# Kernel tuning notes

Hardware: AMD Instinct MI355X
Metric: run time of the kernel (lower is better)

The kernel has to match this reference:

```python
import jax, jax.numpy as jnp
import numpy as np

NEG_BIG = -9e15
ALPHA = 0.2  # LeakyReLU negative slope


def setup_inputs() -> dict:
    key = jax.random.key(0)
    k1, k2, k3, k4 = jax.random.split(key, 4)
    B, N, Fin, Fout = 4, 2048, 128, 128
    h = jax.random.normal(k1, (B, N, Fin), dtype=jnp.float32)
    adj = jax.random.randint(k2, (N, N), 0, 2, dtype=jnp.int32)
    W = jax.random.normal(k3, (Fin, Fout), dtype=jnp.float32) * 0.1
    a = jax.random.normal(k4, (2 * Fout, 1), dtype=jnp.float32) * 0.1
    return {"h": h, "adj": adj, "W": W, "a": a}


def reference(h, adj, W, a):
    # Wh: [B, N, Fout]
    Wh = jnp.einsum('bnf,fo->bno', h, W)
    Fout = W.shape[1]
    a1 = a[:Fout, 0]   # attends to source i
    a2 = a[Fout:, 0]   # attends to target j
    # Decomposed form of leakyrelu(cat([Wh_i, Wh_j]) @ a):
    # e_ij = leakyrelu(a1.Wh_i + a2.Wh_j)  -> [B, N, N]
    f1 = Wh @ a1  # [B, N]
    f2 = Wh @ a2  # [B, N]
    e = jax.nn.leaky_relu(f1[:, :, None] + f2[:, None, :], negative_slope=ALPHA)
    attention = jnp.where(adj[None, :, :] > 0, e, jnp.float32(NEG_BIG))
    attention = jax.nn.softmax(attention, axis=2)
    # dropout is identity in eval mode
    h_prime = jnp.einsum('bij,bjo->bio', attention, Wh)
    return h_prime
```

## Files before the change

### kernel.cpp

```cpp
#include <hip/hip_runtime.h>

#define BB 4
#define NN 2048
#define FF 128
#define NP 2176
#define ALPHA 0.2f
#define SHIFT_C 16.0f

typedef short bf16x8 __attribute__((ext_vector_type(8)));
typedef float f32x4 __attribute__((ext_vector_type(4)));
typedef unsigned u32;

__device__ inline short f2bf(float f) {
    union { float f; unsigned u; } v; v.f = f;
    unsigned r = (v.u + 0x7FFFu + ((v.u >> 16) & 1u)) >> 16;
    return (short)r;
}
__device__ inline float bf2f(short s) {
    union { float f; unsigned u; } v;
    v.u = ((unsigned)(unsigned short)s) << 16;
    return v.f;
}

__device__ inline void cp16(const void* g, void* l) {
    __builtin_amdgcn_global_load_lds(
        (const __attribute__((address_space(1))) u32*)g,
        (__attribute__((address_space(3))) u32*)l, 16, 0, 0);
}

__global__ __launch_bounds__(256) void k_wh(const float* __restrict__ h,
                                            const float* __restrict__ W,
                                            const float* __restrict__ a,
                                            const int* __restrict__ adj,
                                            short* __restrict__ WhHiT,
                                            short* __restrict__ WhLoT,
                                            float* __restrict__ f1,
                                            float* __restrict__ f2,
                                            u32* __restrict__ adjp) {
    __shared__ float Wa[2 * FF];
    __shared__ float hs[16 * 128];
    int tid = threadIdx.x;
    int r0 = blockIdx.x * 16;

    {
        int fin = tid & 127;
        const float* av = (tid < 128) ? a : (a + FF);
        const float* wr = W + (size_t)fin * FF;
        float s = 0.f;
        for (int o = 0; o < FF; o += 4) {
            float4 wv = *(const float4*)(wr + o);
            float4 avv = *(const float4*)(av + o);
            s += wv.x * avv.x + wv.y * avv.y + wv.z * avv.z + wv.w * avv.w;
        }
        Wa[(tid < 128 ? 0 : FF) + fin] = s;
    }
    {
        const float4* src = (const float4*)(h + (size_t)r0 * FF);
        float4* dst = (float4*)hs;
        dst[tid] = src[tid];
        dst[256 + tid] = src[256 + tid];
    }
    {
        int g = blockIdx.x * 256 + tid;
        int row = g >> 6, wd = g & 63;
        const int4* ar = (const int4*)(adj + (size_t)row * NN + wd * 32);
        u32 word = 0;
#pragma unroll
        for (int q = 0; q < 8; ++q) {
            int4 v = ar[q];
            word |= (u32)(v.x > 0) << (q * 4);
            word |= (u32)(v.y > 0) << (q * 4 + 1);
            word |= (u32)(v.z > 0) << (q * 4 + 2);
            word |= (u32)(v.w > 0) << (q * 4 + 3);
        }
        adjp[row * 64 + wd] = word;
    }
    __syncthreads();

    {
        int w = tid >> 6, lane = tid & 63;
        float wa1_0 = Wa[lane], wa1_1 = Wa[lane + 64];
        float wa2_0 = Wa[FF + lane], wa2_1 = Wa[FF + lane + 64];
        for (int rr = 0; rr < 4; ++rr) {
            int rloc = w * 4 + rr;
            int row = r0 + rloc;
            float x0 = hs[rloc * FF + lane], x1 = hs[rloc * FF + lane + 64];
            float s1 = x0 * wa1_0 + x1 * wa1_1;
            float s2 = x0 * wa2_0 + x1 * wa2_1;
#pragma unroll
            for (int m = 32; m >= 1; m >>= 1) {
                s1 += __shfl_xor(s1, m, 64);
                s2 += __shfl_xor(s2, m, 64);
            }
            if (lane == 0) { f1[row] = s1; f2[row] = s2; }
        }
    }

    int f4 = (tid & 31) * 4;
    int rg = tid >> 5;
    float acc[2][4];
#pragma unroll
    for (int rr = 0; rr < 2; ++rr)
#pragma unroll
        for (int cc = 0; cc < 4; ++cc) acc[rr][cc] = 0.f;

    for (int k0 = 0; k0 < FF; k0 += 4) {
        float4 wv[4];
#pragma unroll
        for (int kk = 0; kk < 4; ++kk)
            wv[kk] = *(const float4*)(W + (size_t)(k0 + kk) * FF + f4);
        float4 hv[2];
#pragma unroll
        for (int rr = 0; rr < 2; ++rr)
            hv[rr] = *(const float4*)(hs + (rg * 2 + rr) * FF + k0);
#pragma unroll
        for (int rr = 0; rr < 2; ++rr) {
            float hk[4] = {hv[rr].x, hv[rr].y, hv[rr].z, hv[rr].w};
#pragma unroll
            for (int kk = 0; kk < 4; ++kk) {
                acc[rr][0] += hk[kk] * wv[kk].x;
                acc[rr][1] += hk[kk] * wv[kk].y;
                acc[rr][2] += hk[kk] * wv[kk].z;
                acc[rr][3] += hk[kk] * wv[kk].w;
            }
        }
    }
    int rloc = r0 + rg * 2;
    int b = rloc >> 11;
    int j = rloc & (NN - 1);
#pragma unroll
    for (int cc = 0; cc < 4; ++cc) {
        float v0 = acc[0][cc], v1 = acc[1][cc];
        short h0 = f2bf(v0), h1 = f2bf(v1);
        short l0 = f2bf(v0 - bf2f(h0)), l1 = f2bf(v1 - bf2f(h1));
        size_t off = (size_t)(b * FF + f4 + cc) * NP + j;
        *(short2*)(WhHiT + off) = make_short2(h0, h1);
        *(short2*)(WhLoT + off) = make_short2(l0, l1);
    }
}

__global__ __launch_bounds__(512, 4) void k_attn(const short* __restrict__ WhHiT,
                                                 const short* __restrict__ WhLoT,
                                                 const u32* __restrict__ adjp,
                                                 const float* __restrict__ f1,
                                                 const float* __restrict__ f2,
                                                 float* __restrict__ out) {
    __shared__ __align__(16) char lds[44160];
    char* Bb = lds;
    char* Ab = lds + 32768;
    float* row_ps = (float*)(lds + 43008);
    float* row_inv = (float*)(lds + 44032);

    int tid = threadIdx.x;
    int w = tid >> 6, lane = tid & 63;
    int blk = blockIdx.x;
    int b = blk >> 7;
    int tile = (blk >> 1) & 63;
    int half = blk & 1;
    int i0 = tile * 32;

    int r_a = lane & 15, kg = lane >> 4;
    int mi = w >> 2, ni = w & 3;

    int rb = tid & 31;
    int jp = (tid >> 5) & 15;
    float f1i = f1[b * NN + i0 + rb];
    const u32* aprow = adjp + (size_t)(i0 + rb) * 64;
    const float* f2b = f2 + b * NN;
    int aoff = (rb >> 4) * 1280 + (rb & 15) * 80 + jp * 4;

    int isLo = w >> 2;
    int sub = w & 3;
    int fo_s = half * 64 + sub * 16 + (lane >> 2);
    int oc_s = lane & 3;
    const short* gB = (isLo ? WhLoT : WhHiT) + (size_t)(b * FF + fo_s) * NP + oc_s * 8;
    int bB = isLo * 4096 + sub * 1024;

    f32x4 acc = {0.f, 0.f, 0.f, 0.f};
    float sp = 0.f;

    cp16(gB, Bb + bB);
    cp16(gB + 32, Bb + 8192 + bB);
    {
        float2 qa = *(const float2*)(f2b + jp * 2);
        float2 qb = *(const float2*)(f2b + 32 + jp * 2);
        u32 wa = aprow[0], wb = aprow[1];
        float x;
        x = f1i + qa.x; x = fmaxf(x, ALPHA * x);
        float p00 = __expf(x - SHIFT_C) * (float)((wa >> (jp * 2)) & 1u);
        x = f1i + qa.y; x = fmaxf(x, ALPHA * x);
        float p01 = __expf(x - SHIFT_C) * (float)((wa >> (jp * 2 + 1)) & 1u);
        x = f1i + qb.x; x = fmaxf(x, ALPHA * x);
        float p10 = __expf(x - SHIFT_C) * (float)((wb >> (jp * 2)) & 1u);
        x = f1i + qb.y; x = fmaxf(x, ALPHA * x);
        float p11 = __expf(x - SHIFT_C) * (float)((wb >> (jp * 2 + 1)) & 1u);
        sp += p00 + p01 + p10 + p11;
        union { float f; u32 u; } u0, u1;
        u0.f = p00; u1.f = p01;
        *(u32*)(Ab + aoff) = ((u0.u + 0x8000u) >> 16) | (((u1.u + 0x8000u) >> 16) << 16);
        u0.f = p10; u1.f = p11;
        *(u32*)(Ab + 2560 + aoff) = ((u0.u + 0x8000u) >> 16) | (((u1.u + 0x8000u) >> 16) << 16);
    }
    float2 pfa = *(const float2*)(f2b + 64 + jp * 2);
    float2 pfb = *(const float2*)(f2b + 96 + jp * 2);
    u32 pwa = aprow[2], pwb = aprow[3];
    __syncthreads();

    for (int p = 0; p < 32; ++p) {
        int par = p & 1, opar = par ^ 1;
        {
            int j0n = ((2 * p + 2) & 63) * 32;
            int j1n = ((2 * p + 3) & 63) * 32;
            cp16(gB + j0n, Bb + opar * 16384 + bB);
            cp16(gB + j1n, Bb + opar * 16384 + 8192 + bB);
        }
        {
            float x;
            x = f1i + pfa.x; x = fmaxf(x, ALPHA * x);
            float p00 = __expf(x - SHIFT_C) * (float)((pwa >> (jp * 2)) & 1u);
            x = f1i + pfa.y; x = fmaxf(x, ALPHA * x);
            float p01 = __expf(x - SHIFT_C) * (float)((pwa >> (jp * 2 + 1)) & 1u);
            x = f1i + pfb.x; x = fmaxf(x, ALPHA * x);
            float p10 = __expf(x - SHIFT_C) * (float)((pwb >> (jp * 2)) & 1u);
            x = f1i + pfb.y; x = fmaxf(x, ALPHA * x);
            float p11 = __expf(x - SHIFT_C) * (float)((pwb >> (jp * 2 + 1)) & 1u);
            if (p < 31) sp += p00 + p01 + p10 + p11;
            union { float f; u32 u; } u0, u1;
            u0.f = p00; u1.f = p01;
            *(u32*)(Ab + opar * 5120 + aoff) =
                ((u0.u + 0x8000u) >> 16) | (((u1.u + 0x8000u) >> 16) << 16);
            u0.f = p10; u1.f = p11;
            *(u32*)(Ab + opar * 5120 + 2560 + aoff) =
                ((u0.u + 0x8000u) >> 16) | (((u1.u + 0x8000u) >> 16) << 16);
        }
        {
            int s0 = (2 * p + 4) & 63, s1 = (2 * p + 5) & 63;
            pfa = *(const float2*)(f2b + s0 * 32 + jp * 2);
            pfb = *(const float2*)(f2b + s1 * 32 + jp * 2);
            pwa = aprow[s0]; pwb = aprow[s1];
        }
        {
            char* bbase = Bb + par * 16384;
            char* abase = Ab + par * 5120;
            int boff = (ni * 16 + r_a) * 64 + kg * 16;
            bf16x8 af0 = *(const bf16x8*)(abase + mi * 1280 + r_a * 80 + kg * 16);
            bf16x8 b0h = *(const bf16x8*)(bbase + boff);
            bf16x8 b0l = *(const bf16x8*)(bbase + 4096 + boff);
            acc = __builtin_amdgcn_mfma_f32_16x16x32_bf16(af0, b0h, acc, 0, 0, 0);
            acc = __builtin_amdgcn_mfma_f32_16x16x32_bf16(af0, b0l, acc, 0, 0, 0);
            bf16x8 af1 = *(const bf16x8*)(abase + 2560 + mi * 1280 + r_a * 80 + kg * 16);
            bf16x8 b1h = *(const bf16x8*)(bbase + 8192 + boff);
            bf16x8 b1l = *(const bf16x8*)(bbase + 8192 + 4096 + boff);
            acc = __builtin_amdgcn_mfma_f32_16x16x32_bf16(af1, b1h, acc, 0, 0, 0);
            acc = __builtin_amdgcn_mfma_f32_16x16x32_bf16(af1, b1l, acc, 0, 0, 0);
        }
        __syncthreads();
    }

    sp += __shfl_xor(sp, 32, 64);
    if (lane < 32) row_ps[w * 32 + lane] = sp;
    __syncthreads();
    if (tid < 32) {
        float t = 0.f;
#pragma unroll
        for (int ww = 0; ww < 8; ++ww) t += row_ps[ww * 32 + tid];
        row_inv[tid] = 1.0f / t;
    }
    __syncthreads();

    float* ob = out + ((size_t)b * NN + i0 + mi * 16) * FF + half * 64 + ni * 16;
#pragma unroll
    for (int q = 0; q < 4; ++q) {
        int rr = kg * 4 + q;
        ob[(size_t)rr * FF + r_a] = acc[q] * row_inv[mi * 16 + rr];
    }
}

extern "C" void kernel_launch(void* const* d_in, const int* in_sizes, int n_in,
                              void* d_out, int out_size, void* d_ws, size_t ws_size,
                              hipStream_t stream) {
    const float* h   = (const float*)d_in[0];
    const int*   adj = (const int*)d_in[1];
    const float* W   = (const float*)d_in[2];
    const float* a   = (const float*)d_in[3];
    float* out = (float*)d_out;

    short* WhHiT = (short*)d_ws;
    short* WhLoT = WhHiT + (size_t)BB * FF * NP;
    float* f1 = (float*)(WhLoT + (size_t)BB * FF * NP);
    float* f2 = f1 + (size_t)BB * NN;
    u32* adjp = (u32*)(f2 + (size_t)BB * NN);

    k_wh<<<(BB * NN) / 16, 256, 0, stream>>>(h, W, a, adj, WhHiT, WhLoT, f1, f2, adjp);
    k_attn<<<512, 512, 0, stream>>>(WhHiT, WhLoT, adjp, f1, f2, out);
}
```

Measured before the change: 135.9 us.

## Split MFMA work by K-stage across waves and swizzle B tile LDS layout

Waves are now split by K half (stage) instead of by M row block. Each wave computes both 16-row M blocks for its K half, so every B fragment load feeds two MFMAs, and the two K partial sums are reduced through LDS at the end. The B tile column index is XOR-swizzled on both the global-to-LDS copy and the read side to cut LDS bank conflicts. The cost is an extra accumulator, an LDS partial-sum exchange before the epilogue, and only half the waves doing the output stores.

```diff
diff --git a/kernel.cpp b/kernel.cpp
--- a/kernel.cpp
+++ b/kernel.cpp
@@ -150,6 +150,7 @@
     char* Ab = lds + 32768;
     float* row_ps = (float*)(lds + 43008);
     float* row_inv = (float*)(lds + 44032);
+    float* pP = (float*)lds;
 
     int tid = threadIdx.x;
     int w = tid >> 6, lane = tid & 63;
@@ -160,7 +161,8 @@
     int i0 = tile * 32;
 
     int r_a = lane & 15, kg = lane >> 4;
-    int mi = w >> 2, ni = w & 3;
+    int st = w >> 2, ni = w & 3;
+    int csw = kg ^ ((r_a >> 1) & 3);
 
     int rb = tid & 31;
     int jp = (tid >> 5) & 15;
@@ -172,11 +174,12 @@
     int isLo = w >> 2;
     int sub = w & 3;
     int fo_s = half * 64 + sub * 16 + (lane >> 2);
-    int oc_s = lane & 3;
+    int oc_s = (lane & 3) ^ ((lane >> 3) & 3);
     const short* gB = (isLo ? WhLoT : WhHiT) + (size_t)(b * FF + fo_s) * NP + oc_s * 8;
     int bB = isLo * 4096 + sub * 1024;
 
-    f32x4 acc = {0.f, 0.f, 0.f, 0.f};
+    f32x4 acc0 = {0.f, 0.f, 0.f, 0.f};
+    f32x4 acc1 = {0.f, 0.f, 0.f, 0.f};
     float sp = 0.f;
 
     cp16(gB, Bb + bB);
@@ -240,25 +243,28 @@
             pwa = aprow[s0]; pwb = aprow[s1];
         }
         {
-            char* bbase = Bb + par * 16384;
-            char* abase = Ab + par * 5120;
-            int boff = (ni * 16 + r_a) * 64 + kg * 16;
-            bf16x8 af0 = *(const bf16x8*)(abase + mi * 1280 + r_a * 80 + kg * 16);
-            bf16x8 b0h = *(const bf16x8*)(bbase + boff);
-            bf16x8 b0l = *(const bf16x8*)(bbase + 4096 + boff);
-            acc = __builtin_amdgcn_mfma_f32_16x16x32_bf16(af0, b0h, acc, 0, 0, 0);
-            acc = __builtin_amdgcn_mfma_f32_16x16x32_bf16(af0, b0l, acc, 0, 0, 0);
-            bf16x8 af1 = *(const bf16x8*)(abase + 2560 + mi * 1280 + r_a * 80 + kg * 16);
-            bf16x8 b1h = *(const bf16x8*)(bbase + 8192 + boff);
-            bf16x8 b1l = *(const bf16x8*)(bbase + 8192 + 4096 + boff);
-            acc = __builtin_amdgcn_mfma_f32_16x16x32_bf16(af1, b1h, acc, 0, 0, 0);
-            acc = __builtin_amdgcn_mfma_f32_16x16x32_bf16(af1, b1l, acc, 0, 0, 0);
+            char* bbase = Bb + par * 16384 + st * 8192;
+            char* abase = Ab + par * 5120 + st * 2560;
+            int boff = (ni * 16 + r_a) * 64 + csw * 16;
+            int aoffr = r_a * 80 + kg * 16;
+            bf16x8 a0 = *(const bf16x8*)(abase + aoffr);
+            bf16x8 a1 = *(const bf16x8*)(abase + 1280 + aoffr);
+            bf16x8 bh = *(const bf16x8*)(bbase + boff);
+            bf16x8 bl = *(const bf16x8*)(bbase + 4096 + boff);
+            acc0 = __builtin_amdgcn_mfma_f32_16x16x32_bf16(a0, bh, acc0, 0, 0, 0);
+            acc1 = __builtin_amdgcn_mfma_f32_16x16x32_bf16(a1, bh, acc1, 0, 0, 0);
+            acc0 = __builtin_amdgcn_mfma_f32_16x16x32_bf16(a0, bl, acc0, 0, 0, 0);
+            acc1 = __builtin_amdgcn_mfma_f32_16x16x32_bf16(a1, bl, acc1, 0, 0, 0);
         }
         __syncthreads();
     }
 
     sp += __shfl_xor(sp, 32, 64);
     if (lane < 32) row_ps[w * 32 + lane] = sp;
+    if (st == 0) {
+        *(f32x4*)(pP + (ni * 2 + 0) * 256 + lane * 4) = acc0;
+        *(f32x4*)(pP + (ni * 2 + 1) * 256 + lane * 4) = acc1;
+    }
     __syncthreads();
     if (tid < 32) {
         float t = 0.f;
@@ -268,11 +274,17 @@
     }
     __syncthreads();
 
-    float* ob = out + ((size_t)b * NN + i0 + mi * 16) * FF + half * 64 + ni * 16;
-#pragma unroll
-    for (int q = 0; q < 4; ++q) {
-        int rr = kg * 4 + q;
-        ob[(size_t)rr * FF + r_a] = acc[q] * row_inv[mi * 16 + rr];
+    if (st == 1) {
+        acc0 += *(const f32x4*)(pP + (ni * 2 + 0) * 256 + lane * 4);
+        acc1 += *(const f32x4*)(pP + (ni * 2 + 1) * 256 + lane * 4);
+        float* ob = out + ((size_t)b * NN + i0) * FF + half * 64 + ni * 16;
+#pragma unroll
+        for (int q = 0; q < 4; ++q) {
+            int rr0 = kg * 4 + q;
+            ob[(size_t)rr0 * FF + r_a] = acc0[q] * row_inv[rr0];
+            int rr1 = 16 + kg * 4 + q;
+            ob[(size_t)rr1 * FF + r_a] = acc1[q] * row_inv[rr1];
+        }
     }
 }
 
```

New measurement: 136.3 us. About the same (+0.3%).

## Split attention K dimension across waves with register-only loop and LDS reduction

Applied to the files above, without the earlier changes.

Rewrites the attention kernel so each wave owns a contiguous eighth of the j (key) range. It computes its own bf16 probability fragments in registers and loads Wh hi/lo fragments directly from global memory instead of staging them through LDS. This removes the per-iteration __syncthreads and LDS double buffering. The partial accumulators from the 8 waves are written to a swizzled LDS image and summed at the end before normalization. The cost is more registers (8 accumulators), uncoalesced direct global B loads without a prefetch buffer, and a larger LDS footprint that may lower occupancy.

```diff
diff --git a/kernel.cpp b/kernel.cpp
--- a/kernel.cpp
+++ b/kernel.cpp
@@ -20,12 +20,6 @@
     union { float f; unsigned u; } v;
     v.u = ((unsigned)(unsigned short)s) << 16;
     return v.f;
-}
-
-__device__ inline void cp16(const void* g, void* l) {
-    __builtin_amdgcn_global_load_lds(
-        (const __attribute__((address_space(1))) u32*)g,
-        (__attribute__((address_space(3))) u32*)l, 16, 0, 0);
 }
 
 __global__ __launch_bounds__(256) void k_wh(const float* __restrict__ h,
@@ -139,17 +133,18 @@
     }
 }
 
+#define EV(f2v, f1v, wv, bi) ({ float _t = (f1v) + (f2v); float _x = fmaxf(_t, ALPHA * _t); \
+    __expf(_x - SHIFT_C) * (float)(((wv) >> (bi)) & 1u); })
+
 __global__ __launch_bounds__(512, 4) void k_attn(const short* __restrict__ WhHiT,
                                                  const short* __restrict__ WhLoT,
                                                  const u32* __restrict__ adjp,
                                                  const float* __restrict__ f1,
                                                  const float* __restrict__ f2,
                                                  float* __restrict__ out) {
-    __shared__ __align__(16) char lds[44160];
-    char* Bb = lds;
-    char* Ab = lds + 32768;
-    float* row_ps = (float*)(lds + 43008);
-    float* row_inv = (float*)(lds + 44032);
+    __shared__ __align__(16) char lds[66688];
+    float* row_ps = (float*)(lds + 65536);
+    float* row_inv = (float*)(lds + 66560);
 
     int tid = threadIdx.x;
     int w = tid >> 6, lane = tid & 63;
@@ -159,106 +154,110 @@
     int half = blk & 1;
     int i0 = tile * 32;
 
-    int r_a = lane & 15, kg = lane >> 4;
-    int mi = w >> 2, ni = w & 3;
-
-    int rb = tid & 31;
-    int jp = (tid >> 5) & 15;
-    float f1i = f1[b * NN + i0 + rb];
-    const u32* aprow = adjp + (size_t)(i0 + rb) * 64;
+    int r_c = lane & 15, kg = lane >> 4;
+
     const float* f2b = f2 + b * NN;
-    int aoff = (rb >> 4) * 1280 + (rb & 15) * 80 + jp * 4;
-
-    int isLo = w >> 2;
-    int sub = w & 3;
-    int fo_s = half * 64 + sub * 16 + (lane >> 2);
-    int oc_s = lane & 3;
-    const short* gB = (isLo ? WhLoT : WhHiT) + (size_t)(b * FF + fo_s) * NP + oc_s * 8;
-    int bB = isLo * 4096 + sub * 1024;
-
-    f32x4 acc = {0.f, 0.f, 0.f, 0.f};
-    float sp = 0.f;
-
-    cp16(gB, Bb + bB);
-    cp16(gB + 32, Bb + 8192 + bB);
-    {
-        float2 qa = *(const float2*)(f2b + jp * 2);
-        float2 qb = *(const float2*)(f2b + 32 + jp * 2);
-        u32 wa = aprow[0], wb = aprow[1];
-        float x;
-        x = f1i + qa.x; x = fmaxf(x, ALPHA * x);
-        float p00 = __expf(x - SHIFT_C) * (float)((wa >> (jp * 2)) & 1u);
-        x = f1i + qa.y; x = fmaxf(x, ALPHA * x);
-        float p01 = __expf(x - SHIFT_C) * (float)((wa >> (jp * 2 + 1)) & 1u);
-        x = f1i + qb.x; x = fmaxf(x, ALPHA * x);
-        float p10 = __expf(x - SHIFT_C) * (float)((wb >> (jp * 2)) & 1u);
-        x = f1i + qb.y; x = fmaxf(x, ALPHA * x);
-        float p11 = __expf(x - SHIFT_C) * (float)((wb >> (jp * 2 + 1)) & 1u);
-        sp += p00 + p01 + p10 + p11;
-        union { float f; u32 u; } u0, u1;
-        u0.f = p00; u1.f = p01;
-        *(u32*)(Ab + aoff) = ((u0.u + 0x8000u) >> 16) | (((u1.u + 0x8000u) >> 16) << 16);
-        u0.f = p10; u1.f = p11;
-        *(u32*)(Ab + 2560 + aoff) = ((u0.u + 0x8000u) >> 16) | (((u1.u + 0x8000u) >> 16) << 16);
-    }
-    float2 pfa = *(const float2*)(f2b + 64 + jp * 2);
-    float2 pfb = *(const float2*)(f2b + 96 + jp * 2);
-    u32 pwa = aprow[2], pwb = aprow[3];
-    __syncthreads();
-
-    for (int p = 0; p < 32; ++p) {
-        int par = p & 1, opar = par ^ 1;
+    float f10 = f1[b * NN + i0 + r_c];
+    float f11 = f1[b * NN + i0 + 16 + r_c];
+    const u32* ap0 = adjp + (size_t)(i0 + r_c) * 64;
+    const u32* ap1 = adjp + (size_t)(i0 + 16 + r_c) * 64;
+
+    const ptrdiff_t dLo = (ptrdiff_t)BB * FF * NP;
+    int s0 = w * 8;
+    const short* pB0 = WhHiT + (size_t)(b * FF + half * 64 + 0 * 16 + r_c) * NP + s0 * 32 + kg * 8;
+    const short* pB1 = WhHiT + (size_t)(b * FF + half * 64 + 1 * 16 + r_c) * NP + s0 * 32 + kg * 8;
+    const short* pB2 = WhHiT + (size_t)(b * FF + half * 64 + 2 * 16 + r_c) * NP + s0 * 32 + kg * 8;
+    const short* pB3 = WhHiT + (size_t)(b * FF + half * 64 + 3 * 16 + r_c) * NP + s0 * 32 + kg * 8;
+
+    f32x4 acc0_0 = {0,0,0,0}, acc0_1 = {0,0,0,0};
+    f32x4 acc1_0 = {0,0,0,0}, acc1_1 = {0,0,0,0};
+    f32x4 acc2_0 = {0,0,0,0}, acc2_1 = {0,0,0,0};
+    f32x4 acc3_0 = {0,0,0,0}, acc3_1 = {0,0,0,0};
+    float sp0 = 0.f, sp1 = 0.f;
+
+    float4 q0 = *(const float4*)(f2b + s0 * 32 + kg * 8);
+    float4 q1 = *(const float4*)(f2b + s0 * 32 + kg * 8 + 4);
+    u32 w0 = ap0[s0], w1 = ap1[s0];
+
+#pragma unroll
+    for (int s8 = 0; s8 < 8; ++s8) {
+        bf16x8 bh0 = *(const bf16x8*)(pB0); bf16x8 bl0 = *(const bf16x8*)(pB0 + dLo);
+        bf16x8 bh1 = *(const bf16x8*)(pB1); bf16x8 bl1 = *(const bf16x8*)(pB1 + dLo);
+        bf16x8 bh2 = *(const bf16x8*)(pB2); bf16x8 bl2 = *(const bf16x8*)(pB2 + dLo);
+        bf16x8 bh3 = *(const bf16x8*)(pB3); bf16x8 bl3 = *(const bf16x8*)(pB3 + dLo);
+        int sn = (s0 + s8 + 1) & 63;
+        float4 nq0 = *(const float4*)(f2b + sn * 32 + kg * 8);
+        float4 nq1 = *(const float4*)(f2b + sn * 32 + kg * 8 + 4);
+        u32 nw0 = ap0[sn], nw1 = ap1[sn];
+
+        union { u32 u[4]; bf16x8 v; } A0, A1;
+        int bb = kg * 8;
         {
-            int j0n = ((2 * p + 2) & 63) * 32;
-            int j1n = ((2 * p + 3) & 63) * 32;
-            cp16(gB + j0n, Bb + opar * 16384 + bB);
-            cp16(gB + j1n, Bb + opar * 16384 + 8192 + bB);
-        }
-        {
-            float x;
-            x = f1i + pfa.x; x = fmaxf(x, ALPHA * x);
-            float p00 = __expf(x - SHIFT_C) * (float)((pwa >> (jp * 2)) & 1u);
-            x = f1i + pfa.y; x = fmaxf(x, ALPHA * x);
-            float p01 = __expf(x - SHIFT_C) * (float)((pwa >> (jp * 2 + 1)) & 1u);
-            x = f1i + pfb.x; x = fmaxf(x, ALPHA * x);
-            float p10 = __expf(x - SHIFT_C) * (float)((pwb >> (jp * 2)) & 1u);
-            x = f1i + pfb.y; x = fmaxf(x, ALPHA * x);
-            float p11 = __expf(x - SHIFT_C) * (float)((pwb >> (jp * 2 + 1)) & 1u);
-            if (p < 31) sp += p00 + p01 + p10 + p11;
-            union { float f; u32 u; } u0, u1;
-            u0.f = p00; u1.f = p01;
-            *(u32*)(Ab + opar * 5120 + aoff) =
-                ((u0.u + 0x8000u) >> 16) | (((u1.u + 0x8000u) >> 16) << 16);
-            u0.f = p10; u1.f = p11;
-            *(u32*)(Ab + opar * 5120 + 2560 + aoff) =
-                ((u0.u + 0x8000u) >> 16) | (((u1.u + 0x8000u) >> 16) << 16);
-        }
-        {
-            int s0 = (2 * p + 4) & 63, s1 = (2 * p + 5) & 63;
-            pfa = *(const float2*)(f2b + s0 * 32 + jp * 2);
-            pfb = *(const float2*)(f2b + s1 * 32 + jp * 2);
-            pwa = aprow[s0]; pwb = aprow[s1];
-        }
-        {
-            char* bbase = Bb + par * 16384;
-            char* abase = Ab + par * 5120;
-            int boff = (ni * 16 + r_a) * 64 + kg * 16;
-            bf16x8 af0 = *(const bf16x8*)(abase + mi * 1280 + r_a * 80 + kg * 16);
-            bf16x8 b0h = *(const bf16x8*)(bbase + boff);
-            bf16x8 b0l = *(const bf16x8*)(bbase + 4096 + boff);
-            acc = __builtin_amdgcn_mfma_f32_16x16x32_bf16(af0, b0h, acc, 0, 0, 0);
-            acc = __builtin_amdgcn_mfma_f32_16x16x32_bf16(af0, b0l, acc, 0, 0, 0);
-            bf16x8 af1 = *(const bf16x8*)(abase + 2560 + mi * 1280 + r_a * 80 + kg * 16);
-            bf16x8 b1h = *(const bf16x8*)(bbase + 8192 + boff);
-            bf16x8 b1l = *(const bf16x8*)(bbase + 8192 + 4096 + boff);
-            acc = __builtin_amdgcn_mfma_f32_16x16x32_bf16(af1, b1h, acc, 0, 0, 0);
-            acc = __builtin_amdgcn_mfma_f32_16x16x32_bf16(af1, b1l, acc, 0, 0, 0);
-        }
-        __syncthreads();
-    }
-
-    sp += __shfl_xor(sp, 32, 64);
-    if (lane < 32) row_ps[w * 32 + lane] = sp;
+            float pa, pb;
+            pa = EV(q0.x, f10, w0, bb + 0); pb = EV(q0.y, f10, w0, bb + 1);
+            sp0 += pa + pb;
+            asm("v_cvt_pk_bf16_f32 %0, %1, %2" : "=v"(A0.u[0]) : "v"(pa), "v"(pb));
+            pa = EV(q0.z, f10, w0, bb + 2); pb = EV(q0.w, f10, w0, bb + 3);
+            sp0 += pa + pb;
+            asm("v_cvt_pk_bf16_f32 %0, %1, %2" : "=v"(A0.u[1]) : "v"(pa), "v"(pb));
+            pa = EV(q1.x, f10, w0, bb + 4); pb = EV(q1.y, f10, w0, bb + 5);
+            sp0 += pa + pb;
+            asm("v_cvt_pk_bf16_f32 %0, %1, %2" : "=v"(A0.u[2]) : "v"(pa), "v"(pb));
+            pa = EV(q1.z, f10, w0, bb + 6); pb = EV(q1.w, f10, w0, bb + 7);
+            sp0 += pa + pb;
+            asm("v_cvt_pk_bf16_f32 %0, %1, %2" : "=v"(A0.u[3]) : "v"(pa), "v"(pb));
+
+            pa = EV(q0.x, f11, w1, bb + 0); pb = EV(q0.y, f11, w1, bb + 1);
+            sp1 += pa + pb;
+            asm("v_cvt_pk_bf16_f32 %0, %1, %2" : "=v"(A1.u[0]) : "v"(pa), "v"(pb));
+            pa = EV(q0.z, f11, w1, bb + 2); pb = EV(q0.w, f11, w1, bb + 3);
+            sp1 += pa + pb;
+            asm("v_cvt_pk_bf16_f32 %0, %1, %2" : "=v"(A1.u[1]) : "v"(pa), "v"(pb));
+            pa = EV(q1.x, f11, w1, bb + 4); pb = EV(q1.y, f11, w1, bb + 5);
+            sp1 += pa + pb;
+            asm("v_cvt_pk_bf16_f32 %0, %1, %2" : "=v"(A1.u[2]) : "v"(pa), "v"(pb));
+            pa = EV(q1.z, f11, w1, bb + 6); pb = EV(q1.w, f11, w1, bb + 7);
+            sp1 += pa + pb;
+            asm("v_cvt_pk_bf16_f32 %0, %1, %2" : "=v"(A1.u[3]) : "v"(pa), "v"(pb));
+        }
+
+        acc0_0 = __builtin_amdgcn_mfma_f32_16x16x32_bf16(A0.v, bh0, acc0_0, 0, 0, 0);
+        acc0_0 = __builtin_amdgcn_mfma_f32_16x16x32_bf16(A0.v, bl0, acc0_0, 0, 0, 0);
+        acc0_1 = __builtin_amdgcn_mfma_f32_16x16x32_bf16(A1.v, bh0, acc0_1, 0, 0, 0);
+        acc0_1 = __builtin_amdgcn_mfma_f32_16x16x32_bf16(A1.v, bl0, acc0_1, 0, 0, 0);
+        acc1_0 = __builtin_amdgcn_mfma_f32_16x16x32_bf16(A0.v, bh1, acc1_0, 0, 0, 0);
+        acc1_0 = __builtin_amdgcn_mfma_f32_16x16x32_bf16(A0.v, bl1, acc1_0, 0, 0, 0);
+        acc1_1 = __builtin_amdgcn_mfma_f32_16x16x32_bf16(A1.v, bh1, acc1_1, 0, 0, 0);
+        acc1_1 = __builtin_amdgcn_mfma_f32_16x16x32_bf16(A1.v, bl1, acc1_1, 0, 0, 0);
+        acc2_0 = __builtin_amdgcn_mfma_f32_16x16x32_bf16(A0.v, bh2, acc2_0, 0, 0, 0);
+        acc2_0 = __builtin_amdgcn_mfma_f32_16x16x32_bf16(A0.v, bl2, acc2_0, 0, 0, 0);
+        acc2_1 = __builtin_amdgcn_mfma_f32_16x16x32_bf16(A1.v, bh2, acc2_1, 0, 0, 0);
+        acc2_1 = __builtin_amdgcn_mfma_f32_16x16x32_bf16(A1.v, bl2, acc2_1, 0, 0, 0);
+        acc3_0 = __builtin_amdgcn_mfma_f32_16x16x32_bf16(A0.v, bh3, acc3_0, 0, 0, 0);
+        acc3_0 = __builtin_amdgcn_mfma_f32_16x16x32_bf16(A0.v, bl3, acc3_0, 0, 0, 0);
+        acc3_1 = __builtin_amdgcn_mfma_f32_16x16x32_bf16(A1.v, bh3, acc3_1, 0, 0, 0);
+        acc3_1 = __builtin_amdgcn_mfma_f32_16x16x32_bf16(A1.v, bl3, acc3_1, 0, 0, 0);
+
+        pB0 += 32; pB1 += 32; pB2 += 32; pB3 += 32;
+        q0 = nq0; q1 = nq1; w0 = nw0; w1 = nw1;
+    }
+
+    sp0 += __shfl_xor(sp0, 16, 64); sp0 += __shfl_xor(sp0, 32, 64);
+    sp1 += __shfl_xor(sp1, 16, 64); sp1 += __shfl_xor(sp1, 32, 64);
+    if (lane < 16) {
+        row_ps[w * 32 + lane] = sp0;
+        row_ps[w * 32 + 16 + lane] = sp1;
+    }
+    {
+        char* img = lds + w * 8192;
+#define STACC(NI, MI, A) { int ch = (((NI)*16 + r_c) * 8 + (MI)*4 + kg) ^ (r_c & 7); \
+                           *(f32x4*)(img + ch * 16) = (A); }
+        STACC(0, 0, acc0_0) STACC(0, 1, acc0_1)
+        STACC(1, 0, acc1_0) STACC(1, 1, acc1_1)
+        STACC(2, 0, acc2_0) STACC(2, 1, acc2_1)
+        STACC(3, 0, acc3_0) STACC(3, 1, acc3_1)
+#undef STACC
+    }
     __syncthreads();
     if (tid < 32) {
         float t = 0.f;
@@ -268,11 +267,19 @@
     }
     __syncthreads();
 
-    float* ob = out + ((size_t)b * NN + i0 + mi * 16) * FF + half * 64 + ni * 16;
-#pragma unroll
-    for (int q = 0; q < 4; ++q) {
-        int rr = kg * 4 + q;
-        ob[(size_t)rr * FF + r_a] = acc[q] * row_inv[mi * 16 + rr];
+    {
+        int colg = w * 8 + (lane >> 3);
+        int rq = lane & 7;
+        int ch = (colg * 8 + rq) ^ (colg & 7);
+        f32x4 v = {0, 0, 0, 0};
+#pragma unroll
+        for (int im = 0; im < 8; ++im)
+            v += *(const f32x4*)(lds + im * 8192 + ch * 16);
+        f32x4 rinv = *(const f32x4*)((char*)row_inv + rq * 16);
+        float* ob = out + ((size_t)b * NN + i0 + rq * 4) * FF + half * 64 + colg;
+#pragma unroll
+        for (int q = 0; q < 4; ++q)
+            ob[(size_t)q * FF] = v[q] * rinv[q];
     }
 }
 
```

New measurement: 129.2 us. 1.05x faster.
